# Optimization experiments

Measured on AMD Instinct MI355X. Metric: run time of the kernel, lower is better.

Reference implementation:

```python
import jax, jax.numpy as jnp
import numpy as np

NEG_SLOPE = 0.2
EPS = 1e-16


def setup_inputs() -> dict:
    N, E, IN, H, C = 100000, 1600000, 128, 4, 16
    key = jax.random.key(0)
    k1, k2, k3, k4, k5 = jax.random.split(key, 5)
    x = jax.random.normal(k1, (N, IN), dtype=jnp.float32)
    edge_index = jax.random.randint(k2, (2, E), 0, N, dtype=jnp.int64)
    # Xavier-uniform init like nn.init.xavier_uniform_
    limW = float(np.sqrt(6.0 / (IN + H * C)))
    W = jax.random.uniform(k3, (IN, H * C), dtype=jnp.float32, minval=-limW, maxval=limW)
    lima = float(np.sqrt(6.0 / (H + C)))
    att = jax.random.uniform(k4, (1, H, C), dtype=jnp.float32, minval=-lima, maxval=lima)
    bias = jnp.zeros((H * C,), dtype=jnp.float32)
    return {"x": x, "edge_index": edge_index, "W": W, "att": att, "bias": bias}


def reference(x, edge_index, W, att, bias):
    N = x.shape[0]
    H, C = att.shape[1], att.shape[2]
    h = (x @ W).reshape(N, H, C)  # [N,H,C]
    # add self loops
    loops = jnp.arange(N, dtype=edge_index.dtype)
    row = jnp.concatenate([edge_index[0], loops])  # target nodes
    col = jnp.concatenate([edge_index[1], loops])  # source nodes
    x_i = h[row]  # [Etot,H,C]
    x_j = h[col]
    e = jax.nn.leaky_relu(x_i + x_j, NEG_SLOPE)
    alpha = jnp.einsum('ehc,hc->eh', e, att[0])  # [Etot,H]
    # segment softmax keyed by row (every node has a self loop -> no empty segments)
    amax = jax.lax.stop_gradient(jax.ops.segment_max(alpha, row, num_segments=N))
    ea = jnp.exp(alpha - amax[row])
    denom = jax.ops.segment_sum(ea, row, num_segments=N)
    alpha = ea / (denom[row] + EPS)
    # weighted message scatter-add (dropout p=0 / eval mode)
    out = jax.ops.segment_sum(x_j * alpha[:, :, None], row, num_segments=N)  # [N,H,C]
    out = out.reshape(N, H * C) + bias  # concat=True
    return out
```

## Files before the change

### kernel.cpp

```cpp
#include <hip/hip_runtime.h>

#define NEG_SLOPE 0.2f

typedef float f32x4 __attribute__((ext_vector_type(4)));
typedef short bf16x8 __attribute__((ext_vector_type(8)));

__device__ __forceinline__ unsigned short f2bf(float f) {
  union { float f; unsigned u; } v; v.f = f;
  unsigned r = v.u + 0x7fff + ((v.u >> 16) & 1);
  return (unsigned short)(r >> 16);
}
__device__ __forceinline__ float bf2f(unsigned short u) {
  union { unsigned u; float f; } v; v.u = ((unsigned)u) << 16;
  return v.f;
}
__device__ __forceinline__ unsigned pkbf(float a, float b) {
  return (unsigned)f2bf(a) | ((unsigned)f2bf(b) << 16);
}
__device__ __forceinline__ f32x4 upk4(unsigned ux, unsigned uy) {
  union { unsigned u; float f; } a, b, c, d;
  a.u = ux << 16; b.u = ux & 0xffff0000u;
  c.u = uy << 16; d.u = uy & 0xffff0000u;
  f32x4 r; r.x = a.f; r.y = b.f; r.z = c.f; r.w = d.f;
  return r;
}
__device__ __forceinline__ f32x4 absfma(f32x4 s, f32x4 coef, f32x4 d) {
  d.x = fmaf(fabsf(s.x), coef.x, d.x);
  d.y = fmaf(fabsf(s.y), coef.y, d.y);
  d.z = fmaf(fabsf(s.z), coef.z, d.z);
  d.w = fmaf(fabsf(s.w), coef.w, d.w);
  return d;
}
__device__ __forceinline__ float dpp_xor1_add(float x) {
  int y = __builtin_amdgcn_mov_dpp(__builtin_bit_cast(int, x), 0xB1, 0xF, 0xF, true);
  return x + __builtin_bit_cast(float, y);
}
__device__ __forceinline__ float dpp_xor2_add(float x) {
  int y = __builtin_amdgcn_mov_dpp(__builtin_bit_cast(int, x), 0x4E, 0xF, 0xF, true);
  return x + __builtin_bit_cast(float, y);
}

__global__ __launch_bounds__(256) void gemm_mfma(const float* __restrict__ x,
                                                 const float* __restrict__ W,
                                                 unsigned short* __restrict__ hb, int N) {
  __shared__ uint4 Bl[1024];
  const int t = threadIdx.x;
  {
    const int l = t & 63;
    const int kt = (t >> 6) & 3;
    const int kb = kt * 32 + ((l >> 4) * 8);
    const int cb = l & 15;
#pragma unroll
    for (int ct = 0; ct < 4; ct++) {
      const float* wp = W + (size_t)kb * 64 + ct * 16 + cb;
      unsigned p[4];
#pragma unroll
      for (int jj = 0; jj < 4; jj++)
        p[jj] = pkbf(wp[(2 * jj) * 64], wp[(2 * jj + 1) * 64]);
      Bl[(ct * 4 + kt) * 64 + l] = make_uint4(p[0], p[1], p[2], p[3]);
    }
  }
  __syncthreads();
  const int l = t & 63;
  const int wv = t >> 6;
  union BU { bf16x8 v; uint4 q; };
  BU b[4][4];
#pragma unroll
  for (int ct = 0; ct < 4; ct++)
#pragma unroll
    for (int kt = 0; kt < 4; kt++) b[ct][kt].q = Bl[(ct * 4 + kt) * 64 + l];

  const int rowbase0 = blockIdx.x * 256 + wv * 64;
#pragma unroll
  for (int rt = 0; rt < 4; rt++) {
    const int rbase = rowbase0 + rt * 16;
    int rl = rbase + (l & 15);
    if (rl >= N) rl = N - 1;
    const float* xp = x + (size_t)rl * 128 + ((l >> 4) * 8);
    BU ah[4], alo[4];
#pragma unroll
    for (int kt = 0; kt < 4; kt++) {
      float f[8];
      float4 v0 = *(const float4*)(xp + kt * 32);
      float4 v1 = *(const float4*)(xp + kt * 32 + 4);
      f[0] = v0.x; f[1] = v0.y; f[2] = v0.z; f[3] = v0.w;
      f[4] = v1.x; f[5] = v1.y; f[6] = v1.z; f[7] = v1.w;
      unsigned short hs[8], ls[8];
#pragma unroll
      for (int j = 0; j < 8; j++) {
        hs[j] = f2bf(f[j]);
        ls[j] = f2bf(f[j] - bf2f(hs[j]));
      }
      ah[kt].q = make_uint4(hs[0] | (hs[1] << 16), hs[2] | (hs[3] << 16),
                            hs[4] | (hs[5] << 16), hs[6] | (hs[7] << 16));
      alo[kt].q = make_uint4(ls[0] | (ls[1] << 16), ls[2] | (ls[3] << 16),
                             ls[4] | (ls[5] << 16), ls[6] | (ls[7] << 16));
    }
#pragma unroll
    for (int ct = 0; ct < 4; ct++) {
      f32x4 acc = {0.f, 0.f, 0.f, 0.f};
#pragma unroll
      for (int kt = 0; kt < 4; kt++) {
        acc = __builtin_amdgcn_mfma_f32_16x16x32_bf16(ah[kt].v, b[ct][kt].v, acc, 0, 0, 0);
        acc = __builtin_amdgcn_mfma_f32_16x16x32_bf16(alo[kt].v, b[ct][kt].v, acc, 0, 0, 0);
      }
#pragma unroll
      for (int j = 0; j < 4; j++) {
        float v = acc[j];
        float pv = __shfl_xor(v, 1);
        int row = rbase + (l >> 4) * 4 + j;
        if (!(l & 1) && row < N) {
          *(unsigned*)((char*)hb + (size_t)row * 128 + ct * 32 + (l & 15) * 2) =
              pkbf(v, pv);
        }
      }
    }
  }
}

#define TILE 4096
#define EPT 16
#define NBKT_MAX 256

__global__ __launch_bounds__(256) void bucket_pass(const int* __restrict__ rowi,
                                                   const int* __restrict__ coli,
                                                   int* __restrict__ bucket_fill,
                                                   unsigned* __restrict__ bucket_arr,
                                                   int E, int Cedge, int Ctot, int NBKT) {
  __shared__ int cnt[NBKT_MAX];
  __shared__ int excl[NBKT_MAX];
  __shared__ int gadj[NBKT_MAX];
  __shared__ int tmp[NBKT_MAX];
  __shared__ unsigned staged[TILE];
  __shared__ unsigned char bkof[TILE];
  const int t = threadIdx.x;
  const int tile0 = blockIdx.x * TILE;
  const int nt = min(TILE, E - tile0);
  cnt[t] = 0;
  __syncthreads();
  unsigned pk[EPT];
  int bk[EPT];
#pragma unroll
  for (int j = 0; j < EPT; j++) {
    int i = tile0 + j * 256 + t;
    if (i < E) {
      int r = rowi[i];
      int c = coli[i];
      bk[j] = r >> 9;
      pk[j] = ((unsigned)(r & 511) << 17) | (unsigned)c;
      atomicAdd(&cnt[bk[j]], 1);
    } else {
      bk[j] = -1;
    }
  }
  __syncthreads();
  int v = cnt[t];
  tmp[t] = v;
  __syncthreads();
  for (int off = 1; off < 256; off <<= 1) {
    int val = tmp[t] + ((t >= off) ? tmp[t - off] : 0);
    __syncthreads();
    tmp[t] = val;
    __syncthreads();
  }
  int ex = tmp[t] - v;
  excl[t] = ex;
  int ga = 0;
  if (v > 0) ga = atomicAdd(&bucket_fill[t], v);
  gadj[t] = ga - ex;
  cnt[t] = ex;
  __syncthreads();
#pragma unroll
  for (int j = 0; j < EPT; j++) {
    if (bk[j] >= 0) {
      int lp = atomicAdd(&cnt[bk[j]], 1);
      staged[lp] = pk[j];
      bkof[lp] = (unsigned char)bk[j];
    }
  }
  __syncthreads();
  for (int i = t; i < nt; i += 256) {
    int b = bkof[i];
    int pb = i + gadj[b];
    if (pb < Cedge) bucket_arr[b * Ctot + pb] = staged[i];
  }
}

#define STAGE_CAP 10240

__global__ __launch_bounds__(1024) void csr_pass(unsigned* __restrict__ bucket_arr,
                                                 const int* __restrict__ bucket_fill,
                                                 int2* __restrict__ rowinfo,
                                                 int Cedge, int Ctot, int N) {
  __shared__ unsigned stage[STAGE_CAP];
  __shared__ int hist[512], excl[512], pairs[256];
  const int t = threadIdx.x;
  const int b = blockIdx.x;
  const int bb = b * Ctot;
  const int r0 = b << 9;
  const int nb = min(bucket_fill[b], Cedge);
  for (int i = t; i < 512; i += 1024) hist[i] = ((r0 + i) < N) ? 1 : 0;
  for (int i = t; i < nb; i += 1024) stage[i] = bucket_arr[bb + i];
  __syncthreads();
  for (int i = t; i < nb; i += 1024) atomicAdd(&hist[stage[i] >> 17], 1);
  __syncthreads();
  int h0 = 0, h1 = 0, ps = 0;
  if (t < 256) {
    h0 = hist[2 * t];
    h1 = hist[2 * t + 1];
    ps = h0 + h1;
    pairs[t] = ps;
  }
  __syncthreads();
  for (int off = 1; off < 256; off <<= 1) {
    int val = 0;
    if (t < 256) val = pairs[t] + ((t >= off) ? pairs[t - off] : 0);
    __syncthreads();
    if (t < 256) pairs[t] = val;
    __syncthreads();
  }
  if (t < 256) {
    int pexcl = pairs[t] - ps;
    excl[2 * t] = pexcl;
    excl[2 * t + 1] = pexcl + h0;
  }
  __syncthreads();
  for (int r = t; r < 512; r += 1024) {
    int gr = r0 + r;
    if (gr < N) {
      int o = bb + excl[r];
      rowinfo[gr] = make_int2(o, o + hist[r]);
    }
  }
  __syncthreads();
  for (int i = t; i < nb; i += 1024) {
    unsigned pk = stage[i];
    int r = pk >> 17;
    int lp = atomicAdd(&excl[r], 1);
    bucket_arr[bb + lp] = (pk & 0x1FFFFu) << 7;
  }
  __syncthreads();
  for (int r = t; r < 512; r += 1024) {
    int gr = r0 + r;
    if (gr < N) bucket_arr[bb + excl[r]] = (unsigned)gr << 7;
  }
}

#define ESTEP(u)                                        \
  {                                                     \
    f32x4 jv = upk4((u).x, (u).y);                      \
    f32x4 s = hiv + jv;                                 \
    f32x4 d = s * attA;                                 \
    d = absfma(s, attB, d);                             \
    float al = (d.x + d.y) + (d.z + d.w);               \
    al = dpp_xor1_add(al);                              \
    al = dpp_xor2_add(al);                              \
    float p = __expf(al);                               \
    acc += jv * p;                                      \
    den += p;                                           \
  }

__global__ __launch_bounds__(256) void node_pass(const unsigned short* __restrict__ hb,
                                                 const int2* __restrict__ rowinfo,
                                                 const unsigned* __restrict__ srcs,
                                                 const float* __restrict__ att,
                                                 const float* __restrict__ bias,
                                                 float* __restrict__ out, int N) {
  int w = (blockIdx.x * blockDim.x + threadIdx.x) >> 6;
  if (w >= N) return;
  const int lane = threadIdx.x & 63;
  const int lr = lane & 15;
  const int q = lane >> 4;
  const char* hbc = (const char*)hb;
  const unsigned loff = (unsigned)(lr << 3);
  const f32x4 attv = *(const f32x4*)(att + 4 * lr);
  const f32x4 attA = attv * 0.6f;
  const f32x4 attB = attv * 0.4f;
  const int2 oi = rowinfo[w];
  int k = oi.x;
  const int k1 = oi.y;
  uint2 hu = *(const uint2*)(hbc + (((unsigned)w << 7) | loff));
  const f32x4 hiv = upk4(hu.x, hu.y);
  f32x4 acc = {0.f, 0.f, 0.f, 0.f};
  float den = 0.f;
  unsigned s0, s1, s2, s3;
  if (k + 16 <= k1) {
    s0 = srcs[k + q];
    s1 = srcs[k + 4 + q];
    s2 = srcs[k + 8 + q];
    s3 = srcs[k + 12 + q];
  }
  for (; k + 32 <= k1; k += 16) {
    unsigned n0 = srcs[k + 16 + q];
    unsigned n1 = srcs[k + 20 + q];
    unsigned n2 = srcs[k + 24 + q];
    unsigned n3 = srcs[k + 28 + q];
    uint2 u0 = *(const uint2*)(hbc + (s0 | loff));
    uint2 u1 = *(const uint2*)(hbc + (s1 | loff));
    uint2 u2 = *(const uint2*)(hbc + (s2 | loff));
    uint2 u3 = *(const uint2*)(hbc + (s3 | loff));
    ESTEP(u0);
    ESTEP(u1);
    ESTEP(u2);
    ESTEP(u3);
    s0 = n0; s1 = n1; s2 = n2; s3 = n3;
  }
  if (k + 16 <= k1) {
    uint2 u0 = *(const uint2*)(hbc + (s0 | loff));
    uint2 u1 = *(const uint2*)(hbc + (s1 | loff));
    uint2 u2 = *(const uint2*)(hbc + (s2 | loff));
    uint2 u3 = *(const uint2*)(hbc + (s3 | loff));
    ESTEP(u0);
    ESTEP(u1);
    ESTEP(u2);
    ESTEP(u3);
    k += 16;
  }
  for (; k + 4 <= k1; k += 4) {
    unsigned o = srcs[k + q] | loff;
    uint2 u = *(const uint2*)(hbc + o);
    ESTEP(u);
  }
  if (k < k1) {
    int kk = k + q;
    bool act = kk < k1;
    unsigned o = (act ? srcs[kk] : srcs[k]) | loff;
    uint2 u = *(const uint2*)(hbc + o);
    f32x4 jv = upk4(u.x, u.y);
    f32x4 s = hiv + jv;
    f32x4 d = s * attA;
    d = absfma(s, attB, d);
    float al = (d.x + d.y) + (d.z + d.w);
    al = dpp_xor1_add(al);
    al = dpp_xor2_add(al);
    float p = act ? __expf(al) : 0.f;
    acc += jv * p;
    den += p;
  }
  acc.x += __shfl_xor(acc.x, 16); acc.y += __shfl_xor(acc.y, 16);
  acc.z += __shfl_xor(acc.z, 16); acc.w += __shfl_xor(acc.w, 16);
  den += __shfl_xor(den, 16);
  acc.x += __shfl_xor(acc.x, 32); acc.y += __shfl_xor(acc.y, 32);
  acc.z += __shfl_xor(acc.z, 32); acc.w += __shfl_xor(acc.w, 32);
  den += __shfl_xor(den, 32);
  if (q == 0) {
    float inv = 1.0f / (den + 1e-16f);
    f32x4 bv = *(const f32x4*)(bias + 4 * lr);
    f32x4 o = acc * inv + bv;
    *(f32x4*)(out + (size_t)w * 64 + 4 * lr) = o;
  }
}

extern "C" void kernel_launch(void* const* d_in, const int* in_sizes, int n_in,
                              void* d_out, int out_size, void* d_ws, size_t ws_size,
                              hipStream_t stream) {
  const float* x = (const float*)d_in[0];
  const int* eidx = (const int*)d_in[1];
  const float* W = (const float*)d_in[2];
  const float* att = (const float*)d_in[3];
  const float* bias = (const float*)d_in[4];
  float* out = (float*)d_out;

  const int N = in_sizes[0] / 128;
  const int E = in_sizes[1] / 2;
  const int NBKT = (N + 511) >> 9;
  int Cedge = (E + NBKT - 1) / NBKT;
  Cedge = Cedge + Cedge / 8 + 64;
  Cedge = (Cedge + 15) & ~15;
  if (Cedge > STAGE_CAP) Cedge = STAGE_CAP;
  const int Ctot = Cedge + 512;

  unsigned short* hb = (unsigned short*)d_ws;
  int* bucket_fill = (int*)(hb + (size_t)N * 64);
  int2* rowinfo = (int2*)(bucket_fill + NBKT_MAX);
  unsigned* bucket_arr = (unsigned*)(rowinfo + N);

  hipMemsetAsync(bucket_fill, 0, NBKT_MAX * sizeof(int), stream);

  gemm_mfma<<<(N + 255) / 256, 256, 0, stream>>>(x, W, hb, N);
  bucket_pass<<<(E + TILE - 1) / TILE, 256, 0, stream>>>(eidx, eidx + E, bucket_fill,
                                                         bucket_arr, E, Cedge, Ctot, NBKT);
  csr_pass<<<NBKT, 1024, 0, stream>>>(bucket_arr, bucket_fill, rowinfo, Cedge, Ctot, N);
  node_pass<<<(N * 64 + 255) / 256, 256, 0, stream>>>(hb, rowinfo, bucket_arr, att, bias,
                                                      out, N);
}
```

Before: 114.4 us.

## Merge GEMM and bucketing into one launch; process two nodes per wavefront

The GEMM and edge-bucketing kernels become two block roles of a single launch that share a union shared-memory buffer, so the two independent stages run concurrently and one launch is saved. The node aggregation kernel now has each wavefront handle two destination nodes with interleaved gather loops. This exposes more independent loads per wave but uses half as many waves. The shared buffer is sized to the larger role, which may lower occupancy for the GEMM blocks, and the paired loops add register pressure and imbalance when two nodes have different degrees.

New measurement: 101.0 us. 11.7% less time.

```diff
diff --git a/kernel.cpp b/kernel.cpp
--- a/kernel.cpp
+++ b/kernel.cpp
@@ -40,10 +40,16 @@
   return x + __builtin_bit_cast(float, y);
 }
 
-__global__ __launch_bounds__(256) void gemm_mfma(const float* __restrict__ x,
-                                                 const float* __restrict__ W,
-                                                 unsigned short* __restrict__ hb, int N) {
-  __shared__ uint4 Bl[1024];
+#define TILE 4096
+#define EPT 16
+#define NBKT_MAX 256
+#define SMEM_BYTES 24576
+
+__device__ __forceinline__ void gemm_role(const float* __restrict__ x,
+                                          const float* __restrict__ W,
+                                          unsigned short* __restrict__ hb, int N,
+                                          char* smem, int bid) {
+  uint4* Bl = (uint4*)smem;
   const int t = threadIdx.x;
   {
     const int l = t & 63;
@@ -70,7 +76,7 @@
 #pragma unroll
     for (int kt = 0; kt < 4; kt++) b[ct][kt].q = Bl[(ct * 4 + kt) * 64 + l];
 
-  const int rowbase0 = blockIdx.x * 256 + wv * 64;
+  const int rowbase0 = bid * 256 + wv * 64;
 #pragma unroll
   for (int rt = 0; rt < 4; rt++) {
     const int rbase = rowbase0 + rt * 16;
@@ -118,23 +124,19 @@
   }
 }
 
-#define TILE 4096
-#define EPT 16
-#define NBKT_MAX 256
-
-__global__ __launch_bounds__(256) void bucket_pass(const int* __restrict__ rowi,
-                                                   const int* __restrict__ coli,
-                                                   int* __restrict__ bucket_fill,
-                                                   unsigned* __restrict__ bucket_arr,
-                                                   int E, int Cedge, int Ctot, int NBKT) {
-  __shared__ int cnt[NBKT_MAX];
-  __shared__ int excl[NBKT_MAX];
-  __shared__ int gadj[NBKT_MAX];
-  __shared__ int tmp[NBKT_MAX];
-  __shared__ unsigned staged[TILE];
-  __shared__ unsigned char bkof[TILE];
+__device__ __forceinline__ void bucket_role(const int* __restrict__ rowi,
+                                            const int* __restrict__ coli,
+                                            int* __restrict__ bucket_fill,
+                                            unsigned* __restrict__ bucket_arr, int E,
+                                            int Cedge, int Ctot, int NBKT, char* smem,
+                                            int bid) {
+  int* cnt = (int*)smem;
+  int* gadj = cnt + 256;
+  int* tmp = gadj + 256;
+  unsigned* staged = (unsigned*)(tmp + 256);
+  unsigned char* bkof = (unsigned char*)(staged + TILE);
   const int t = threadIdx.x;
-  const int tile0 = blockIdx.x * TILE;
+  const int tile0 = bid * TILE;
   const int nt = min(TILE, E - tile0);
   cnt[t] = 0;
   __syncthreads();
@@ -164,7 +166,6 @@
     __syncthreads();
   }
   int ex = tmp[t] - v;
-  excl[t] = ex;
   int ga = 0;
   if (v > 0) ga = atomicAdd(&bucket_fill[t], v);
   gadj[t] = ga - ex;
@@ -184,6 +185,23 @@
     int pb = i + gadj[b];
     if (pb < Cedge) bucket_arr[b * Ctot + pb] = staged[i];
   }
+}
+
+__global__ __launch_bounds__(256) void gemm_bucket(const float* __restrict__ x,
+                                                   const float* __restrict__ W,
+                                                   unsigned short* __restrict__ hb, int N,
+                                                   const int* __restrict__ rowi,
+                                                   const int* __restrict__ coli,
+                                                   int* __restrict__ bucket_fill,
+                                                   unsigned* __restrict__ bucket_arr,
+                                                   int E, int Cedge, int Ctot, int NBKT,
+                                                   int G1) {
+  __shared__ __align__(16) char smem[SMEM_BYTES];
+  if ((int)blockIdx.x < G1)
+    gemm_role(x, W, hb, N, smem, blockIdx.x);
+  else
+    bucket_role(rowi, coli, bucket_fill, bucket_arr, E, Cedge, Ctot, NBKT, smem,
+                blockIdx.x - G1);
 }
 
 #define STAGE_CAP 10240
@@ -246,18 +264,18 @@
   }
 }
 
-#define ESTEP(u)                                        \
+#define ESTEPN(hivX, accX, denX, u)                     \
   {                                                     \
     f32x4 jv = upk4((u).x, (u).y);                      \
-    f32x4 s = hiv + jv;                                 \
+    f32x4 s = hivX + jv;                                \
     f32x4 d = s * attA;                                 \
     d = absfma(s, attB, d);                             \
     float al = (d.x + d.y) + (d.z + d.w);               \
     al = dpp_xor1_add(al);                              \
     al = dpp_xor2_add(al);                              \
     float p = __expf(al);                               \
-    acc += jv * p;                                      \
-    den += p;                                           \
+    accX += jv * p;                                     \
+    denX += p;                                          \
   }
 
 __global__ __launch_bounds__(256) void node_pass(const unsigned short* __restrict__ hb,
@@ -266,8 +284,12 @@
                                                  const float* __restrict__ att,
                                                  const float* __restrict__ bias,
                                                  float* __restrict__ out, int N) {
-  int w = (blockIdx.x * blockDim.x + threadIdx.x) >> 6;
-  if (w >= N) return;
+  const int wp = (blockIdx.x * blockDim.x + threadIdx.x) >> 6;
+  const int a = wp * 2;
+  if (a >= N) return;
+  const int bn = a + 1;
+  const bool bvalid = bn < N;
+  const int bc = bvalid ? bn : a;
   const int lane = threadIdx.x & 63;
   const int lr = lane & 15;
   const int q = lane >> 4;
@@ -276,78 +298,111 @@
   const f32x4 attv = *(const f32x4*)(att + 4 * lr);
   const f32x4 attA = attv * 0.6f;
   const f32x4 attB = attv * 0.4f;
-  const int2 oi = rowinfo[w];
-  int k = oi.x;
-  const int k1 = oi.y;
-  uint2 hu = *(const uint2*)(hbc + (((unsigned)w << 7) | loff));
-  const f32x4 hiv = upk4(hu.x, hu.y);
-  f32x4 acc = {0.f, 0.f, 0.f, 0.f};
-  float den = 0.f;
-  unsigned s0, s1, s2, s3;
-  if (k + 16 <= k1) {
-    s0 = srcs[k + q];
-    s1 = srcs[k + 4 + q];
-    s2 = srcs[k + 8 + q];
-    s3 = srcs[k + 12 + q];
-  }
-  for (; k + 32 <= k1; k += 16) {
-    unsigned n0 = srcs[k + 16 + q];
-    unsigned n1 = srcs[k + 20 + q];
-    unsigned n2 = srcs[k + 24 + q];
-    unsigned n3 = srcs[k + 28 + q];
-    uint2 u0 = *(const uint2*)(hbc + (s0 | loff));
-    uint2 u1 = *(const uint2*)(hbc + (s1 | loff));
-    uint2 u2 = *(const uint2*)(hbc + (s2 | loff));
-    uint2 u3 = *(const uint2*)(hbc + (s3 | loff));
-    ESTEP(u0);
-    ESTEP(u1);
-    ESTEP(u2);
-    ESTEP(u3);
-    s0 = n0; s1 = n1; s2 = n2; s3 = n3;
-  }
-  if (k + 16 <= k1) {
-    uint2 u0 = *(const uint2*)(hbc + (s0 | loff));
-    uint2 u1 = *(const uint2*)(hbc + (s1 | loff));
-    uint2 u2 = *(const uint2*)(hbc + (s2 | loff));
-    uint2 u3 = *(const uint2*)(hbc + (s3 | loff));
-    ESTEP(u0);
-    ESTEP(u1);
-    ESTEP(u2);
-    ESTEP(u3);
-    k += 16;
-  }
-  for (; k + 4 <= k1; k += 4) {
-    unsigned o = srcs[k + q] | loff;
+  const int2 ria = rowinfo[a];
+  const int2 rib = rowinfo[bc];
+  uint2 hua = *(const uint2*)(hbc + (((unsigned)a << 7) | loff));
+  uint2 hub = *(const uint2*)(hbc + (((unsigned)bc << 7) | loff));
+  const f32x4 hivA = upk4(hua.x, hua.y);
+  const f32x4 hivB = upk4(hub.x, hub.y);
+  int ka = ria.x, kb = rib.x;
+  const int ka1 = ria.y;
+  const int kb1 = bvalid ? rib.y : rib.x;
+  f32x4 accA = {0.f, 0.f, 0.f, 0.f};
+  f32x4 accB = {0.f, 0.f, 0.f, 0.f};
+  float denA = 0.f, denB = 0.f;
+  while (ka + 8 <= ka1 && kb + 8 <= kb1) {
+    unsigned oa0 = srcs[ka + q] | loff;
+    unsigned oa1 = srcs[ka + 4 + q] | loff;
+    unsigned ob0 = srcs[kb + q] | loff;
+    unsigned ob1 = srcs[kb + 4 + q] | loff;
+    uint2 ua0 = *(const uint2*)(hbc + oa0);
+    uint2 ua1 = *(const uint2*)(hbc + oa1);
+    uint2 ub0 = *(const uint2*)(hbc + ob0);
+    uint2 ub1 = *(const uint2*)(hbc + ob1);
+    ESTEPN(hivA, accA, denA, ua0);
+    ESTEPN(hivA, accA, denA, ua1);
+    ESTEPN(hivB, accB, denB, ub0);
+    ESTEPN(hivB, accB, denB, ub1);
+    ka += 8;
+    kb += 8;
+  }
+  for (; ka + 8 <= ka1; ka += 8) {
+    unsigned o0 = srcs[ka + q] | loff;
+    unsigned o1 = srcs[ka + 4 + q] | loff;
+    uint2 u0 = *(const uint2*)(hbc + o0);
+    uint2 u1 = *(const uint2*)(hbc + o1);
+    ESTEPN(hivA, accA, denA, u0);
+    ESTEPN(hivA, accA, denA, u1);
+  }
+  for (; kb + 8 <= kb1; kb += 8) {
+    unsigned o0 = srcs[kb + q] | loff;
+    unsigned o1 = srcs[kb + 4 + q] | loff;
+    uint2 u0 = *(const uint2*)(hbc + o0);
+    uint2 u1 = *(const uint2*)(hbc + o1);
+    ESTEPN(hivB, accB, denB, u0);
+    ESTEPN(hivB, accB, denB, u1);
+  }
+  for (; ka + 4 <= ka1; ka += 4) {
+    unsigned o = srcs[ka + q] | loff;
     uint2 u = *(const uint2*)(hbc + o);
-    ESTEP(u);
-  }
-  if (k < k1) {
-    int kk = k + q;
-    bool act = kk < k1;
-    unsigned o = (act ? srcs[kk] : srcs[k]) | loff;
+    ESTEPN(hivA, accA, denA, u);
+  }
+  for (; kb + 4 <= kb1; kb += 4) {
+    unsigned o = srcs[kb + q] | loff;
+    uint2 u = *(const uint2*)(hbc + o);
+    ESTEPN(hivB, accB, denB, u);
+  }
+  if (ka < ka1) {
+    bool act = (ka + q) < ka1;
+    unsigned o = (act ? srcs[ka + q] : srcs[ka]) | loff;
     uint2 u = *(const uint2*)(hbc + o);
     f32x4 jv = upk4(u.x, u.y);
-    f32x4 s = hiv + jv;
+    f32x4 s = hivA + jv;
     f32x4 d = s * attA;
     d = absfma(s, attB, d);
     float al = (d.x + d.y) + (d.z + d.w);
     al = dpp_xor1_add(al);
     al = dpp_xor2_add(al);
     float p = act ? __expf(al) : 0.f;
-    acc += jv * p;
-    den += p;
-  }
-  acc.x += __shfl_xor(acc.x, 16); acc.y += __shfl_xor(acc.y, 16);
-  acc.z += __shfl_xor(acc.z, 16); acc.w += __shfl_xor(acc.w, 16);
-  den += __shfl_xor(den, 16);
-  acc.x += __shfl_xor(acc.x, 32); acc.y += __shfl_xor(acc.y, 32);
-  acc.z += __shfl_xor(acc.z, 32); acc.w += __shfl_xor(acc.w, 32);
-  den += __shfl_xor(den, 32);
+    accA += jv * p;
+    denA += p;
+  }
+  if (kb < kb1) {
+    bool act = (kb + q) < kb1;
+    unsigned o = (act ? srcs[kb + q] : srcs[kb]) | loff;
+    uint2 u = *(const uint2*)(hbc + o);
+    f32x4 jv = upk4(u.x, u.y);
+    f32x4 s = hivB + jv;
+    f32x4 d = s * attA;
+    d = absfma(s, attB, d);
+    float al = (d.x + d.y) + (d.z + d.w);
+    al = dpp_xor1_add(al);
+    al = dpp_xor2_add(al);
+    float p = act ? __expf(al) : 0.f;
+    accB += jv * p;
+    denB += p;
+  }
+#pragma unroll
+  for (int j = 0; j < 4; j++) {
+    accA[j] += __shfl_xor(accA[j], 16);
+    accB[j] += __shfl_xor(accB[j], 16);
+    accA[j] += __shfl_xor(accA[j], 32);
+    accB[j] += __shfl_xor(accB[j], 32);
+  }
+  denA += __shfl_xor(denA, 16);
+  denB += __shfl_xor(denB, 16);
+  denA += __shfl_xor(denA, 32);
+  denB += __shfl_xor(denB, 32);
   if (q == 0) {
-    float inv = 1.0f / (den + 1e-16f);
-    f32x4 bv = *(const f32x4*)(bias + 4 * lr);
-    f32x4 o = acc * inv + bv;
-    *(f32x4*)(out + (size_t)w * 64 + 4 * lr) = o;
+    const f32x4 bv = *(const f32x4*)(bias + 4 * lr);
+    float invA = 1.0f / (denA + 1e-16f);
+    f32x4 oa = accA * invA + bv;
+    *(f32x4*)(out + (size_t)a * 64 + 4 * lr) = oa;
+    if (bvalid) {
+      float invB = 1.0f / (denB + 1e-16f);
+      f32x4 ob = accB * invB + bv;
+      *(f32x4*)(out + (size_t)bn * 64 + 4 * lr) = ob;
+    }
   }
 }
 
@@ -377,10 +432,12 @@
 
   hipMemsetAsync(bucket_fill, 0, NBKT_MAX * sizeof(int), stream);
 
-  gemm_mfma<<<(N + 255) / 256, 256, 0, stream>>>(x, W, hb, N);
-  bucket_pass<<<(E + TILE - 1) / TILE, 256, 0, stream>>>(eidx, eidx + E, bucket_fill,
-                                                         bucket_arr, E, Cedge, Ctot, NBKT);
+  const int G1 = (N + 255) / 256;
+  const int G2 = (E + TILE - 1) / TILE;
+  gemm_bucket<<<G1 + G2, 256, 0, stream>>>(x, W, hb, N, eidx, eidx + E, bucket_fill,
+                                           bucket_arr, E, Cedge, Ctot, NBKT, G1);
   csr_pass<<<NBKT, 1024, 0, stream>>>(bucket_arr, bucket_fill, rowinfo, Cedge, Ctot, N);
-  node_pass<<<(N * 64 + 255) / 256, 256, 0, stream>>>(hb, rowinfo, bucket_arr, att, bias,
-                                                      out, N);
-}
+  const int npairs = (N + 1) / 2;
+  node_pass<<<(npairs * 64 + 255) / 256, 256, 0, stream>>>(hb, rowinfo, bucket_arr, att,
+                                                           bias, out, N);
+}
```
